# Kernel tuning notes

Measured on AMD Instinct MI355X. Metric: run time of the kernel, lower is better.

## Reference

```python
import jax, jax.numpy as jnp
import numpy as np

N, H, S = 100, 16, 6  # n_subactors, neurons, state_size
B, T = 128, 128


def setup_inputs() -> dict:
    key = jax.random.key(0)
    ks = jax.random.split(key, 12)
    sc = 1.0 / np.sqrt(H)
    inp = {
        "x":   jax.random.normal(ks[0], (B, T, N, S), dtype=jnp.float32),
        # stacked per-subactor GRU weights (torch gate order: r, z, n)
        "Wih": jax.random.uniform(ks[1], (N, 3 * H, S), minval=-sc, maxval=sc, dtype=jnp.float32),
        "Whh": jax.random.uniform(ks[2], (N, 3 * H, H), minval=-sc, maxval=sc, dtype=jnp.float32),
        "bih": jax.random.uniform(ks[3], (N, 3 * H), minval=-sc, maxval=sc, dtype=jnp.float32),
        "bhh": jax.random.uniform(ks[4], (N, 3 * H), minval=-sc, maxval=sc, dtype=jnp.float32),
        # stacked per-subactor MLP weights
        "W1": jax.random.uniform(ks[5], (N, H, H), minval=-sc, maxval=sc, dtype=jnp.float32),
        "b1": jax.random.uniform(ks[6], (N, H), minval=-sc, maxval=sc, dtype=jnp.float32),
        "W2": jax.random.uniform(ks[7], (N, H, H), minval=-sc, maxval=sc, dtype=jnp.float32),
        "b2": jax.random.uniform(ks[8], (N, H), minval=-sc, maxval=sc, dtype=jnp.float32),
        "W3": jax.random.uniform(ks[9], (N, 1, H), minval=-sc, maxval=sc, dtype=jnp.float32),
        "b3": jax.random.uniform(ks[10], (N, 1), minval=-sc, maxval=sc, dtype=jnp.float32),
    }
    return inp


def reference(x, Wih, Whh, bih, bhh, W1, b1, W2, b2, W3, b3):
    b, t, n, s = x.shape
    h = Whh.shape[-1]
    # input projections for all timesteps/subactors at once: [B,T,N,3H]
    xi = jnp.einsum('btns,ngs->btng', x, Wih) + bih

    def step(hprev, xt):  # hprev [B,N,H], xt [B,N,3H]
        hh = jnp.einsum('bnh,ngh->bng', hprev, Whh) + bhh
        xr, xz, xn = jnp.split(xt, 3, axis=-1)
        hr, hz, hn = jnp.split(hh, 3, axis=-1)
        r = jax.nn.sigmoid(xr + hr)
        z = jax.nn.sigmoid(xz + hz)
        nn_ = jnp.tanh(xn + r * hn)
        hnew = (1.0 - z) * nn_ + z * hprev
        return hnew, hnew

    h0 = jnp.zeros((b, n, h), dtype=x.dtype)
    _, hs = jax.lax.scan(step, h0, jnp.moveaxis(xi, 1, 0))  # [T,B,N,H]
    hs = jnp.moveaxis(hs, 0, 1)  # [B,T,N,H]

    y = jax.nn.relu(jnp.einsum('btnh,nkh->btnk', hs, W1) + b1)
    y = jax.nn.relu(jnp.einsum('btnh,nkh->btnk', y, W2) + b2)
    y = jax.nn.relu(jnp.einsum('btnh,nkh->btnk', y, W3) + b3)  # [B,T,N,1]
    # torch: stack over subactors -> [N,B,T,1] then .view(-1, t, nzones)
    return jnp.transpose(y, (2, 0, 1, 3)).reshape(-1, t, n)
```

## Files before the change

### kernel.cpp

```cpp
#include <hip/hip_runtime.h>

namespace {

constexpr int kN = 100;
constexpr int kH = 16;
constexpr int kS = 6;
constexpr int kB = 128;
constexpr int kT = 128;
constexpr int kNS = kN * kS;
constexpr int kXB = kT * kNS;
constexpr float kL2E = 1.44269504088896340736f;

typedef float f32x4 __attribute__((ext_vector_type(4)));
typedef float vf2 __attribute__((ext_vector_type(2)));
typedef short bf16x8 __attribute__((ext_vector_type(8)));

union Frag {
  unsigned u[4];
  bf16x8 v;
};

__device__ __forceinline__ unsigned pkbf(float a, float b) {
  unsigned ua = __builtin_bit_cast(unsigned, a);
  unsigned ub = __builtin_bit_cast(unsigned, b);
  ua += 0x7fffu + ((ua >> 16) & 1u);
  ub += 0x7fffu + ((ub >> 16) & 1u);
  return (ua >> 16) | (ub & 0xffff0000u);
}

__device__ __forceinline__ float rcp_fast(float v) {
  return __builtin_amdgcn_rcpf(v);
}
__device__ __forceinline__ float exp2_fast(float v) {
  return __builtin_amdgcn_exp2f(v);
}
__device__ __forceinline__ vf2 pkfma(vf2 a, vf2 b, vf2 c) {
  return __builtin_elementwise_fma(a, b, c);
}

__device__ __forceinline__ f32x4 mfma16(bf16x8 a, bf16x8 b, f32x4 c) {
  return __builtin_amdgcn_mfma_f32_16x16x32_bf16(a, b, c, 0, 0, 0);
}

__device__ __forceinline__ void mkA(Frag& F, int qt, const float* hrow,
                                    const float* xrow, float sc) {
  F.u[0] = F.u[1] = F.u[2] = F.u[3] = 0u;
  if (hrow) {
    F.u[0] = pkbf(hrow[4 * qt + 0] * sc, hrow[4 * qt + 1] * sc);
    F.u[1] = pkbf(hrow[4 * qt + 2] * sc, hrow[4 * qt + 3] * sc);
  }
  if (xrow && qt < 3) {
    F.u[2] = pkbf(xrow[2 * qt + 0] * sc, xrow[2 * qt + 1] * sc);
  }
}

}

__global__ __launch_bounds__(64) void actor_pk2(
    const float* __restrict__ x, const float* __restrict__ Wih,
    const float* __restrict__ Whh, const float* __restrict__ bih,
    const float* __restrict__ bhh, const float* __restrict__ W1,
    const float* __restrict__ b1, const float* __restrict__ W2,
    const float* __restrict__ b2, const float* __restrict__ W3,
    const float* __restrict__ b3, float* __restrict__ out) {
  const int tid = (int)threadIdx.x;
  const int j = tid & 15;
  const int qt = tid >> 4;
  const int n = (int)blockIdx.x >> 3;
  const int bt = (int)blockIdx.x & 7;

  Frag Ar, Az, Anh, Anx, Ay1, Ay2;
  mkA(Ar, qt, Whh + ((size_t)n * 48 + j) * 16, Wih + ((size_t)n * 48 + j) * 6,
      kL2E);
  mkA(Az, qt, Whh + ((size_t)n * 48 + 16 + j) * 16,
      Wih + ((size_t)n * 48 + 16 + j) * 6, kL2E);
  mkA(Anh, qt, Whh + ((size_t)n * 48 + 32 + j) * 16, nullptr, 2.0f * kL2E);
  mkA(Anx, qt, nullptr, Wih + ((size_t)n * 48 + 32 + j) * 6, 2.0f * kL2E);
  mkA(Ay1, qt, W1 + ((size_t)n * 16 + j) * 16, nullptr, 1.0f);
  mkA(Ay2, qt, W2 + ((size_t)n * 16 + j) * 16, nullptr, 1.0f);

  f32x4 Cbr, Cbz, Cbhn, Cbin, Cb1, Cb2;
  vf2 w301, w323;
#pragma unroll
  for (int r = 0; r < 4; ++r) {
    const int gi = n * 48 + 4 * qt + r;
    Cbr[r] = (bih[gi] + bhh[gi]) * kL2E;
    Cbz[r] = (bih[gi + 16] + bhh[gi + 16]) * kL2E;
    Cbin[r] = bih[gi + 32] * 2.0f * kL2E;
    Cbhn[r] = bhh[gi + 32] * 2.0f * kL2E;
    const int hi = n * 16 + 4 * qt + r;
    Cb1[r] = b1[hi];
    Cb2[r] = b2[hi];
  }
  w301 = (vf2){W3[n * 16 + 4 * qt + 0], W3[n * 16 + 4 * qt + 1]};
  w323 = (vf2){W3[n * 16 + 4 * qt + 2], W3[n * 16 + 4 * qt + 3]};
  const float b3s = b3[n];

  const int b = bt * 16 + j;
  const float* px =
      x + (size_t)b * kXB + (size_t)n * kS + (qt < 3 ? 2 * qt : 0);
  float* outp = out + ((size_t)n * kB + b) * kT;

  float2 xr[4];
#pragma unroll
  for (int i = 0; i < 4; ++i) xr[i] = *(const float2*)(px + (size_t)i * kNS);

  vf2 hp01 = (vf2){0.f, 0.f}, hp23 = (vf2){0.f, 0.f};
  unsigned P0 = 0u, P1 = 0u;

  const f32x4 zero4 = {0.f, 0.f, 0.f, 0.f};
  f32x4 Cy1p = zero4;
  f32x4 Cy2p = zero4;
  float s4[4] = {0.f, 0.f, 0.f, 0.f};

  const vf2 one2 = (vf2){1.f, 1.f};
  const vf2 m2 = (vf2){-2.f, -2.f};
  const vf2 z2 = (vf2){0.f, 0.f};

  auto step = [&](int t, bool doRec, bool doA, bool doB, bool doC) {
    f32x4 Cr, Cz, Chn, Cxn, Cy1n = Cy1p;
    if (t <= kT) {
      const int sl = t & 3;
      Frag Bf;
      Bf.u[0] = P0;
      Bf.u[1] = P1;
      Bf.u[2] = (qt < 3) ? pkbf(xr[sl].x, xr[sl].y) : 0u;
      Bf.u[3] = 0u;
      {
        int tc = t + 4;
        if (tc > kT - 1) tc = kT - 1;
        xr[sl] = *(const float2*)(px + (size_t)tc * kNS);
      }
      if (doRec) {
        Cr = mfma16(Ar.v, Bf.v, Cbr);
        Cz = mfma16(Az.v, Bf.v, Cbz);
        Chn = mfma16(Anh.v, Bf.v, Cbhn);
        Cxn = mfma16(Anx.v, Bf.v, Cbin);
      }
      Cy1n = mfma16(Ay1.v, Bf.v, Cb1);
    }

    if (doB) {
      vf2 a = __builtin_elementwise_max((vf2){Cy2p[0], Cy2p[1]}, z2);
      vf2 c = __builtin_elementwise_max((vf2){Cy2p[2], Cy2p[3]}, z2);
      vf2 p = pkfma(c, w323, a * w301);
      s4[(t - 3) & 3] = p.x + p.y;
    }

    if (doA) {
      vf2 a = __builtin_elementwise_max((vf2){Cy1p[0], Cy1p[1]}, z2);
      vf2 c = __builtin_elementwise_max((vf2){Cy1p[2], Cy1p[3]}, z2);
      Frag By;
      By.u[0] = pkbf(a.x, a.y);
      By.u[1] = pkbf(c.x, c.y);
      By.u[2] = 0u;
      By.u[3] = 0u;
      Cy2p = mfma16(Ay2.v, By.v, Cb2);
    }

    if (doC) {
      float v0 = s4[0], v1 = s4[1], v2 = s4[2], v3 = s4[3];
      v0 += __shfl_xor(v0, 16);
      v1 += __shfl_xor(v1, 16);
      v2 += __shfl_xor(v2, 16);
      v3 += __shfl_xor(v3, 16);
      v0 += __shfl_xor(v0, 32);
      v1 += __shfl_xor(v1, 32);
      v2 += __shfl_xor(v2, 32);
      v3 += __shfl_xor(v3, 32);
      if (qt == 0) {
        float4 o = {fmaxf(v0 + b3s, 0.f), fmaxf(v1 + b3s, 0.f),
                    fmaxf(v2 + b3s, 0.f), fmaxf(v3 + b3s, 0.f)};
        *(float4*)(outp + (t - 6)) = o;
      }
    }

    if (doRec) {
      vf2 cr01 = {Cr[0], Cr[1]}, cr23 = {Cr[2], Cr[3]};
      vf2 cz01 = {Cz[0], Cz[1]}, cz23 = {Cz[2], Cz[3]};
      vf2 chn01 = {Chn[0], Chn[1]}, chn23 = {Chn[2], Chn[3]};
      vf2 cxn01 = {Cxn[0], Cxn[1]}, cxn23 = {Cxn[2], Cxn[3]};

      vf2 er01 = {exp2_fast(-cr01.x), exp2_fast(-cr01.y)};
      vf2 er23 = {exp2_fast(-cr23.x), exp2_fast(-cr23.y)};
      vf2 dr01 = er01 + one2, dr23 = er23 + one2;
      vf2 rr01 = {rcp_fast(dr01.x), rcp_fast(dr01.y)};
      vf2 rr23 = {rcp_fast(dr23.x), rcp_fast(dr23.y)};

      vf2 ez01 = {exp2_fast(-cz01.x), exp2_fast(-cz01.y)};
      vf2 ez23 = {exp2_fast(-cz23.x), exp2_fast(-cz23.y)};
      vf2 dz01 = ez01 + one2, dz23 = ez23 + one2;
      vf2 zz01 = {rcp_fast(dz01.x), rcp_fast(dz01.y)};
      vf2 zz23 = {rcp_fast(dz23.x), rcp_fast(dz23.y)};

      vf2 np01 = pkfma(rr01, chn01, cxn01);
      vf2 np23 = pkfma(rr23, chn23, cxn23);
      vf2 en01 = {exp2_fast(np01.x), exp2_fast(np01.y)};
      vf2 en23 = {exp2_fast(np23.x), exp2_fast(np23.y)};
      vf2 dn01 = en01 + one2, dn23 = en23 + one2;
      vf2 rn01 = {rcp_fast(dn01.x), rcp_fast(dn01.y)};
      vf2 rn23 = {rcp_fast(dn23.x), rcp_fast(dn23.y)};
      vf2 nn01 = pkfma(m2, rn01, one2);
      vf2 nn23 = pkfma(m2, rn23, one2);

      hp01 = pkfma(zz01, hp01 - nn01, nn01);
      hp23 = pkfma(zz23, hp23 - nn23, nn23);
      P0 = pkbf(hp01.x, hp01.y);
      P1 = pkbf(hp23.x, hp23.y);
    }

    Cy1p = Cy1n;
  };

  step(0, true, false, false, false);
  step(1, true, false, false, false);
  step(2, true, true, false, false);
  step(3, true, true, true, false);

  for (int t4 = 4; t4 < kT; t4 += 4) {
    step(t4 + 0, true, true, true, false);
    step(t4 + 1, true, true, true, false);
    step(t4 + 2, true, true, true, true);
    step(t4 + 3, true, true, true, false);
  }

  step(kT, false, true, true, false);
  step(kT + 1, false, true, true, false);
  step(kT + 2, false, false, true, true);
}

extern "C" void kernel_launch(void* const* d_in, const int* in_sizes, int n_in,
                              void* d_out, int out_size, void* d_ws,
                              size_t ws_size, hipStream_t stream) {
  const float* x = (const float*)d_in[0];
  const float* Wih = (const float*)d_in[1];
  const float* Whh = (const float*)d_in[2];
  const float* bih = (const float*)d_in[3];
  const float* bhh = (const float*)d_in[4];
  const float* W1 = (const float*)d_in[5];
  const float* b1 = (const float*)d_in[6];
  const float* W2 = (const float*)d_in[7];
  const float* b2 = (const float*)d_in[8];
  const float* W3 = (const float*)d_in[9];
  const float* b3 = (const float*)d_in[10];
  float* out = (float*)d_out;

  actor_pk2<<<dim3(kN * 8), dim3(64), 0, stream>>>(x, Wih, Whh, bih, bhh, W1,
                                                   b1, W2, b2, W3, b3, out);
}
```

Baseline: 138.3 us.

## Interleave two subactor GRU recurrences per wavefront to hide dependency latency

Each 64-thread block now processes two subactors (n and n+50) for the same batch tile, interleaving their MFMA and gate computations in one unrolled step. The grid drops from 800 to 400 blocks. The aim is to fill the latency of the serial MFMA→exp/rcp→pack chain with independent work from the second recurrence. In exchange it roughly doubles register use and halves the number of concurrently running waves.

```diff
diff --git a/kernel.cpp b/kernel.cpp
--- a/kernel.cpp
+++ b/kernel.cpp
@@ -56,7 +56,7 @@
 
 }
 
-__global__ __launch_bounds__(64) void actor_pk2(
+__global__ __launch_bounds__(64) void actor_dual(
     const float* __restrict__ x, const float* __restrict__ Wih,
     const float* __restrict__ Whh, const float* __restrict__ bih,
     const float* __restrict__ bhh, const float* __restrict__ W1,
@@ -66,150 +66,176 @@
   const int tid = (int)threadIdx.x;
   const int j = tid & 15;
   const int qt = tid >> 4;
-  const int n = (int)blockIdx.x >> 3;
+  const int np = (int)blockIdx.x >> 3;
   const int bt = (int)blockIdx.x & 7;
 
-  Frag Ar, Az, Anh, Anx, Ay1, Ay2;
-  mkA(Ar, qt, Whh + ((size_t)n * 48 + j) * 16, Wih + ((size_t)n * 48 + j) * 6,
-      kL2E);
-  mkA(Az, qt, Whh + ((size_t)n * 48 + 16 + j) * 16,
-      Wih + ((size_t)n * 48 + 16 + j) * 6, kL2E);
-  mkA(Anh, qt, Whh + ((size_t)n * 48 + 32 + j) * 16, nullptr, 2.0f * kL2E);
-  mkA(Anx, qt, nullptr, Wih + ((size_t)n * 48 + 32 + j) * 6, 2.0f * kL2E);
-  mkA(Ay1, qt, W1 + ((size_t)n * 16 + j) * 16, nullptr, 1.0f);
-  mkA(Ay2, qt, W2 + ((size_t)n * 16 + j) * 16, nullptr, 1.0f);
-
-  f32x4 Cbr, Cbz, Cbhn, Cbin, Cb1, Cb2;
-  vf2 w301, w323;
-#pragma unroll
-  for (int r = 0; r < 4; ++r) {
-    const int gi = n * 48 + 4 * qt + r;
-    Cbr[r] = (bih[gi] + bhh[gi]) * kL2E;
-    Cbz[r] = (bih[gi + 16] + bhh[gi + 16]) * kL2E;
-    Cbin[r] = bih[gi + 32] * 2.0f * kL2E;
-    Cbhn[r] = bhh[gi + 32] * 2.0f * kL2E;
-    const int hi = n * 16 + 4 * qt + r;
-    Cb1[r] = b1[hi];
-    Cb2[r] = b2[hi];
-  }
-  w301 = (vf2){W3[n * 16 + 4 * qt + 0], W3[n * 16 + 4 * qt + 1]};
-  w323 = (vf2){W3[n * 16 + 4 * qt + 2], W3[n * 16 + 4 * qt + 3]};
-  const float b3s = b3[n];
-
-  const int b = bt * 16 + j;
-  const float* px =
-      x + (size_t)b * kXB + (size_t)n * kS + (qt < 3 ? 2 * qt : 0);
-  float* outp = out + ((size_t)n * kB + b) * kT;
-
-  float2 xr[4];
-#pragma unroll
-  for (int i = 0; i < 4; ++i) xr[i] = *(const float2*)(px + (size_t)i * kNS);
-
-  vf2 hp01 = (vf2){0.f, 0.f}, hp23 = (vf2){0.f, 0.f};
-  unsigned P0 = 0u, P1 = 0u;
+  Frag Ar[2], Az[2], Anh[2], Anx[2], Ay1[2], Ay2[2];
+  f32x4 Cbr[2], Cbz[2], Cbhn[2], Cbin[2], Cb1[2], Cb2[2];
+  vf2 w301[2], w323[2];
+  float b3s[2];
+  const float* px[2];
+  float* outp[2];
+
+#pragma unroll
+  for (int c = 0; c < 2; ++c) {
+    const int n = np + 50 * c;
+    mkA(Ar[c], qt, Whh + ((size_t)n * 48 + j) * 16,
+        Wih + ((size_t)n * 48 + j) * 6, kL2E);
+    mkA(Az[c], qt, Whh + ((size_t)n * 48 + 16 + j) * 16,
+        Wih + ((size_t)n * 48 + 16 + j) * 6, kL2E);
+    mkA(Anh[c], qt, Whh + ((size_t)n * 48 + 32 + j) * 16, nullptr,
+        2.0f * kL2E);
+    mkA(Anx[c], qt, nullptr, Wih + ((size_t)n * 48 + 32 + j) * 6,
+        2.0f * kL2E);
+    mkA(Ay1[c], qt, W1 + ((size_t)n * 16 + j) * 16, nullptr, 1.0f);
+    mkA(Ay2[c], qt, W2 + ((size_t)n * 16 + j) * 16, nullptr, 1.0f);
+#pragma unroll
+    for (int r = 0; r < 4; ++r) {
+      const int gi = n * 48 + 4 * qt + r;
+      Cbr[c][r] = (bih[gi] + bhh[gi]) * kL2E;
+      Cbz[c][r] = (bih[gi + 16] + bhh[gi + 16]) * kL2E;
+      Cbin[c][r] = bih[gi + 32] * 2.0f * kL2E;
+      Cbhn[c][r] = bhh[gi + 32] * 2.0f * kL2E;
+      const int hi = n * 16 + 4 * qt + r;
+      Cb1[c][r] = b1[hi];
+      Cb2[c][r] = b2[hi];
+    }
+    w301[c] = (vf2){W3[n * 16 + 4 * qt + 0], W3[n * 16 + 4 * qt + 1]};
+    w323[c] = (vf2){W3[n * 16 + 4 * qt + 2], W3[n * 16 + 4 * qt + 3]};
+    b3s[c] = b3[n];
+    const int b = bt * 16 + j;
+    px[c] = x + (size_t)b * kXB + (size_t)n * kS + (qt < 3 ? 2 * qt : 0);
+    outp[c] = out + ((size_t)n * kB + b) * kT;
+  }
+
+  float2 xr[2][4];
+#pragma unroll
+  for (int c = 0; c < 2; ++c)
+#pragma unroll
+    for (int i = 0; i < 4; ++i)
+      xr[c][i] = *(const float2*)(px[c] + (size_t)i * kNS);
+
+  vf2 hp01[2] = {(vf2){0.f, 0.f}, (vf2){0.f, 0.f}};
+  vf2 hp23[2] = {(vf2){0.f, 0.f}, (vf2){0.f, 0.f}};
+  unsigned P0[2] = {0u, 0u}, P1[2] = {0u, 0u};
 
   const f32x4 zero4 = {0.f, 0.f, 0.f, 0.f};
-  f32x4 Cy1p = zero4;
-  f32x4 Cy2p = zero4;
-  float s4[4] = {0.f, 0.f, 0.f, 0.f};
+  f32x4 Cy1p[2] = {zero4, zero4};
+  f32x4 Cy2p[2] = {zero4, zero4};
+  float s4[2][4] = {{0.f, 0.f, 0.f, 0.f}, {0.f, 0.f, 0.f, 0.f}};
 
   const vf2 one2 = (vf2){1.f, 1.f};
   const vf2 m2 = (vf2){-2.f, -2.f};
   const vf2 z2 = (vf2){0.f, 0.f};
 
   auto step = [&](int t, bool doRec, bool doA, bool doB, bool doC) {
-    f32x4 Cr, Cz, Chn, Cxn, Cy1n = Cy1p;
+    f32x4 Cr[2], Cz[2], Chn[2], Cxn[2], Cy1n[2];
+    Cy1n[0] = Cy1p[0];
+    Cy1n[1] = Cy1p[1];
+
     if (t <= kT) {
       const int sl = t & 3;
-      Frag Bf;
-      Bf.u[0] = P0;
-      Bf.u[1] = P1;
-      Bf.u[2] = (qt < 3) ? pkbf(xr[sl].x, xr[sl].y) : 0u;
-      Bf.u[3] = 0u;
-      {
-        int tc = t + 4;
-        if (tc > kT - 1) tc = kT - 1;
-        xr[sl] = *(const float2*)(px + (size_t)tc * kNS);
-      }
-      if (doRec) {
-        Cr = mfma16(Ar.v, Bf.v, Cbr);
-        Cz = mfma16(Az.v, Bf.v, Cbz);
-        Chn = mfma16(Anh.v, Bf.v, Cbhn);
-        Cxn = mfma16(Anx.v, Bf.v, Cbin);
-      }
-      Cy1n = mfma16(Ay1.v, Bf.v, Cb1);
-    }
-
-    if (doB) {
-      vf2 a = __builtin_elementwise_max((vf2){Cy2p[0], Cy2p[1]}, z2);
-      vf2 c = __builtin_elementwise_max((vf2){Cy2p[2], Cy2p[3]}, z2);
-      vf2 p = pkfma(c, w323, a * w301);
-      s4[(t - 3) & 3] = p.x + p.y;
-    }
-
-    if (doA) {
-      vf2 a = __builtin_elementwise_max((vf2){Cy1p[0], Cy1p[1]}, z2);
-      vf2 c = __builtin_elementwise_max((vf2){Cy1p[2], Cy1p[3]}, z2);
-      Frag By;
-      By.u[0] = pkbf(a.x, a.y);
-      By.u[1] = pkbf(c.x, c.y);
-      By.u[2] = 0u;
-      By.u[3] = 0u;
-      Cy2p = mfma16(Ay2.v, By.v, Cb2);
+#pragma unroll
+      for (int c = 0; c < 2; ++c) {
+        Frag Bf;
+        Bf.u[0] = P0[c];
+        Bf.u[1] = P1[c];
+        Bf.u[2] = (qt < 3) ? pkbf(xr[c][sl].x, xr[c][sl].y) : 0u;
+        Bf.u[3] = 0u;
+        {
+          int tc = t + 4;
+          if (tc > kT - 1) tc = kT - 1;
+          xr[c][sl] = *(const float2*)(px[c] + (size_t)tc * kNS);
+        }
+        if (doRec) {
+          Cr[c] = mfma16(Ar[c].v, Bf.v, Cbr[c]);
+          Cz[c] = mfma16(Az[c].v, Bf.v, Cbz[c]);
+          Chn[c] = mfma16(Anh[c].v, Bf.v, Cbhn[c]);
+          Cxn[c] = mfma16(Anx[c].v, Bf.v, Cbin[c]);
+        }
+        Cy1n[c] = mfma16(Ay1[c].v, Bf.v, Cb1[c]);
+      }
+    }
+
+#pragma unroll
+    for (int c = 0; c < 2; ++c) {
+      if (doB) {
+        vf2 a = __builtin_elementwise_max((vf2){Cy2p[c][0], Cy2p[c][1]}, z2);
+        vf2 d = __builtin_elementwise_max((vf2){Cy2p[c][2], Cy2p[c][3]}, z2);
+        vf2 p = pkfma(d, w323[c], a * w301[c]);
+        s4[c][(t - 3) & 3] = p.x + p.y;
+      }
+      if (doA) {
+        vf2 a = __builtin_elementwise_max((vf2){Cy1p[c][0], Cy1p[c][1]}, z2);
+        vf2 d = __builtin_elementwise_max((vf2){Cy1p[c][2], Cy1p[c][3]}, z2);
+        Frag By;
+        By.u[0] = pkbf(a.x, a.y);
+        By.u[1] = pkbf(d.x, d.y);
+        By.u[2] = 0u;
+        By.u[3] = 0u;
+        Cy2p[c] = mfma16(Ay2[c].v, By.v, Cb2[c]);
+      }
     }
 
     if (doC) {
-      float v0 = s4[0], v1 = s4[1], v2 = s4[2], v3 = s4[3];
-      v0 += __shfl_xor(v0, 16);
-      v1 += __shfl_xor(v1, 16);
-      v2 += __shfl_xor(v2, 16);
-      v3 += __shfl_xor(v3, 16);
-      v0 += __shfl_xor(v0, 32);
-      v1 += __shfl_xor(v1, 32);
-      v2 += __shfl_xor(v2, 32);
-      v3 += __shfl_xor(v3, 32);
-      if (qt == 0) {
-        float4 o = {fmaxf(v0 + b3s, 0.f), fmaxf(v1 + b3s, 0.f),
-                    fmaxf(v2 + b3s, 0.f), fmaxf(v3 + b3s, 0.f)};
-        *(float4*)(outp + (t - 6)) = o;
+#pragma unroll
+      for (int c = 0; c < 2; ++c) {
+        float v0 = s4[c][0], v1 = s4[c][1], v2 = s4[c][2], v3 = s4[c][3];
+        v0 += __shfl_xor(v0, 16);
+        v1 += __shfl_xor(v1, 16);
+        v2 += __shfl_xor(v2, 16);
+        v3 += __shfl_xor(v3, 16);
+        v0 += __shfl_xor(v0, 32);
+        v1 += __shfl_xor(v1, 32);
+        v2 += __shfl_xor(v2, 32);
+        v3 += __shfl_xor(v3, 32);
+        if (qt == 0) {
+          float4 o = {fmaxf(v0 + b3s[c], 0.f), fmaxf(v1 + b3s[c], 0.f),
+                      fmaxf(v2 + b3s[c], 0.f), fmaxf(v3 + b3s[c], 0.f)};
+          *(float4*)(outp[c] + (t - 6)) = o;
+        }
       }
     }
 
     if (doRec) {
-      vf2 cr01 = {Cr[0], Cr[1]}, cr23 = {Cr[2], Cr[3]};
-      vf2 cz01 = {Cz[0], Cz[1]}, cz23 = {Cz[2], Cz[3]};
-      vf2 chn01 = {Chn[0], Chn[1]}, chn23 = {Chn[2], Chn[3]};
-      vf2 cxn01 = {Cxn[0], Cxn[1]}, cxn23 = {Cxn[2], Cxn[3]};
-
-      vf2 er01 = {exp2_fast(-cr01.x), exp2_fast(-cr01.y)};
-      vf2 er23 = {exp2_fast(-cr23.x), exp2_fast(-cr23.y)};
-      vf2 dr01 = er01 + one2, dr23 = er23 + one2;
-      vf2 rr01 = {rcp_fast(dr01.x), rcp_fast(dr01.y)};
-      vf2 rr23 = {rcp_fast(dr23.x), rcp_fast(dr23.y)};
-
-      vf2 ez01 = {exp2_fast(-cz01.x), exp2_fast(-cz01.y)};
-      vf2 ez23 = {exp2_fast(-cz23.x), exp2_fast(-cz23.y)};
-      vf2 dz01 = ez01 + one2, dz23 = ez23 + one2;
-      vf2 zz01 = {rcp_fast(dz01.x), rcp_fast(dz01.y)};
-      vf2 zz23 = {rcp_fast(dz23.x), rcp_fast(dz23.y)};
-
-      vf2 np01 = pkfma(rr01, chn01, cxn01);
-      vf2 np23 = pkfma(rr23, chn23, cxn23);
-      vf2 en01 = {exp2_fast(np01.x), exp2_fast(np01.y)};
-      vf2 en23 = {exp2_fast(np23.x), exp2_fast(np23.y)};
-      vf2 dn01 = en01 + one2, dn23 = en23 + one2;
-      vf2 rn01 = {rcp_fast(dn01.x), rcp_fast(dn01.y)};
-      vf2 rn23 = {rcp_fast(dn23.x), rcp_fast(dn23.y)};
-      vf2 nn01 = pkfma(m2, rn01, one2);
-      vf2 nn23 = pkfma(m2, rn23, one2);
-
-      hp01 = pkfma(zz01, hp01 - nn01, nn01);
-      hp23 = pkfma(zz23, hp23 - nn23, nn23);
-      P0 = pkbf(hp01.x, hp01.y);
-      P1 = pkbf(hp23.x, hp23.y);
-    }
-
-    Cy1p = Cy1n;
+#pragma unroll
+      for (int c = 0; c < 2; ++c) {
+        vf2 cr01 = {Cr[c][0], Cr[c][1]}, cr23 = {Cr[c][2], Cr[c][3]};
+        vf2 cz01 = {Cz[c][0], Cz[c][1]}, cz23 = {Cz[c][2], Cz[c][3]};
+        vf2 chn01 = {Chn[c][0], Chn[c][1]}, chn23 = {Chn[c][2], Chn[c][3]};
+        vf2 cxn01 = {Cxn[c][0], Cxn[c][1]}, cxn23 = {Cxn[c][2], Cxn[c][3]};
+
+        vf2 er01 = {exp2_fast(-cr01.x), exp2_fast(-cr01.y)};
+        vf2 er23 = {exp2_fast(-cr23.x), exp2_fast(-cr23.y)};
+        vf2 dr01 = er01 + one2, dr23 = er23 + one2;
+        vf2 rr01 = {rcp_fast(dr01.x), rcp_fast(dr01.y)};
+        vf2 rr23 = {rcp_fast(dr23.x), rcp_fast(dr23.y)};
+
+        vf2 ez01 = {exp2_fast(-cz01.x), exp2_fast(-cz01.y)};
+        vf2 ez23 = {exp2_fast(-cz23.x), exp2_fast(-cz23.y)};
+        vf2 dz01 = ez01 + one2, dz23 = ez23 + one2;
+        vf2 zz01 = {rcp_fast(dz01.x), rcp_fast(dz01.y)};
+        vf2 zz23 = {rcp_fast(dz23.x), rcp_fast(dz23.y)};
+
+        vf2 np01 = pkfma(rr01, chn01, cxn01);
+        vf2 np23 = pkfma(rr23, chn23, cxn23);
+        vf2 en01 = {exp2_fast(np01.x), exp2_fast(np01.y)};
+        vf2 en23 = {exp2_fast(np23.x), exp2_fast(np23.y)};
+        vf2 dn01 = en01 + one2, dn23 = en23 + one2;
+        vf2 rn01 = {rcp_fast(dn01.x), rcp_fast(dn01.y)};
+        vf2 rn23 = {rcp_fast(dn23.x), rcp_fast(dn23.y)};
+        vf2 nn01 = pkfma(m2, rn01, one2);
+        vf2 nn23 = pkfma(m2, rn23, one2);
+
+        hp01[c] = pkfma(zz01, hp01[c] - nn01, nn01);
+        hp23[c] = pkfma(zz23, hp23[c] - nn23, nn23);
+        P0[c] = pkbf(hp01[c].x, hp01[c].y);
+        P1[c] = pkbf(hp23[c].x, hp23[c].y);
+      }
+    }
+
+    Cy1p[0] = Cy1n[0];
+    Cy1p[1] = Cy1n[1];
   };
 
   step(0, true, false, false, false);
@@ -245,6 +271,6 @@
   const float* b3 = (const float*)d_in[10];
   float* out = (float*)d_out;
 
-  actor_pk2<<<dim3(kN * 8), dim3(64), 0, stream>>>(x, Wih, Whh, bih, bhh, W1,
-                                                   b1, W2, b2, W3, b3, out);
-}
+  actor_dual<<<dim3(50 * 8), dim3(64), 0, stream>>>(x, Wih, Whh, bih, bhh, W1,
+                                                    b1, W2, b2, W3, b3, out);
+}
```

After: 179.7 us. +29.9%, slower.

## Split GRU recurrence and MLP head into producer/consumer wavefronts via LDS

Applied to the files above, without the earlier changes.

The single-wave kernel becomes a two-wave block. Wave 0 runs only the serial GRU recurrence over chunks of 8 timesteps and writes the packed bf16 hidden states into a 16-slot LDS ring. Wave 1 consumes the previous chunk and runs the three-layer MLP and the output reduction. A block barrier is placed after each chunk. The aim is to take the MLP MFMAs and shuffles off the latency-critical recurrence path so the two waves can overlap, and to prefetch x 8 steps ahead with double buffering. The cost is a barrier every 8 steps, LDS traffic, and twice as many threads per block.

```diff
diff --git a/kernel.cpp b/kernel.cpp
--- a/kernel.cpp
+++ b/kernel.cpp
@@ -13,6 +13,7 @@
 
 typedef float f32x4 __attribute__((ext_vector_type(4)));
 typedef float vf2 __attribute__((ext_vector_type(2)));
+typedef unsigned u32x2 __attribute__((ext_vector_type(2)));
 typedef short bf16x8 __attribute__((ext_vector_type(8)));
 
 union Frag {
@@ -56,177 +57,184 @@
 
 }
 
-__global__ __launch_bounds__(64) void actor_pk2(
+__global__ __launch_bounds__(128) void actor_pc(
     const float* __restrict__ x, const float* __restrict__ Wih,
     const float* __restrict__ Whh, const float* __restrict__ bih,
     const float* __restrict__ bhh, const float* __restrict__ W1,
     const float* __restrict__ b1, const float* __restrict__ W2,
     const float* __restrict__ b2, const float* __restrict__ W3,
     const float* __restrict__ b3, float* __restrict__ out) {
+  __shared__ unsigned shh[16 * 128];
+
   const int tid = (int)threadIdx.x;
-  const int j = tid & 15;
-  const int qt = tid >> 4;
+  const int wid = tid >> 6;
+  const int lane = tid & 63;
+  const int j = lane & 15;
+  const int qt = lane >> 4;
   const int n = (int)blockIdx.x >> 3;
   const int bt = (int)blockIdx.x & 7;
-
-  Frag Ar, Az, Anh, Anx, Ay1, Ay2;
-  mkA(Ar, qt, Whh + ((size_t)n * 48 + j) * 16, Wih + ((size_t)n * 48 + j) * 6,
-      kL2E);
-  mkA(Az, qt, Whh + ((size_t)n * 48 + 16 + j) * 16,
-      Wih + ((size_t)n * 48 + 16 + j) * 6, kL2E);
-  mkA(Anh, qt, Whh + ((size_t)n * 48 + 32 + j) * 16, nullptr, 2.0f * kL2E);
-  mkA(Anx, qt, nullptr, Wih + ((size_t)n * 48 + 32 + j) * 6, 2.0f * kL2E);
-  mkA(Ay1, qt, W1 + ((size_t)n * 16 + j) * 16, nullptr, 1.0f);
-  mkA(Ay2, qt, W2 + ((size_t)n * 16 + j) * 16, nullptr, 1.0f);
-
-  f32x4 Cbr, Cbz, Cbhn, Cbin, Cb1, Cb2;
-  vf2 w301, w323;
-#pragma unroll
-  for (int r = 0; r < 4; ++r) {
-    const int gi = n * 48 + 4 * qt + r;
-    Cbr[r] = (bih[gi] + bhh[gi]) * kL2E;
-    Cbz[r] = (bih[gi + 16] + bhh[gi + 16]) * kL2E;
-    Cbin[r] = bih[gi + 32] * 2.0f * kL2E;
-    Cbhn[r] = bhh[gi + 32] * 2.0f * kL2E;
-    const int hi = n * 16 + 4 * qt + r;
-    Cb1[r] = b1[hi];
-    Cb2[r] = b2[hi];
-  }
-  w301 = (vf2){W3[n * 16 + 4 * qt + 0], W3[n * 16 + 4 * qt + 1]};
-  w323 = (vf2){W3[n * 16 + 4 * qt + 2], W3[n * 16 + 4 * qt + 3]};
-  const float b3s = b3[n];
-
   const int b = bt * 16 + j;
+
+  Frag Ar, Az, Anh, Anx;
+  f32x4 Cbr, Cbz, Cbhn, Cbin;
   const float* px =
       x + (size_t)b * kXB + (size_t)n * kS + (qt < 3 ? 2 * qt : 0);
+
+  Frag Ay1, Ay2;
+  f32x4 Cb1, Cb2;
+  vf2 w301, w323;
+  float b3s;
   float* outp = out + ((size_t)n * kB + b) * kT;
 
-  float2 xr[4];
-#pragma unroll
-  for (int i = 0; i < 4; ++i) xr[i] = *(const float2*)(px + (size_t)i * kNS);
-
+  if (wid == 0) {
+    mkA(Ar, qt, Whh + ((size_t)n * 48 + j) * 16,
+        Wih + ((size_t)n * 48 + j) * 6, kL2E);
+    mkA(Az, qt, Whh + ((size_t)n * 48 + 16 + j) * 16,
+        Wih + ((size_t)n * 48 + 16 + j) * 6, kL2E);
+    mkA(Anh, qt, Whh + ((size_t)n * 48 + 32 + j) * 16, nullptr, 2.0f * kL2E);
+    mkA(Anx, qt, nullptr, Wih + ((size_t)n * 48 + 32 + j) * 6, 2.0f * kL2E);
+#pragma unroll
+    for (int r = 0; r < 4; ++r) {
+      const int gi = n * 48 + 4 * qt + r;
+      Cbr[r] = (bih[gi] + bhh[gi]) * kL2E;
+      Cbz[r] = (bih[gi + 16] + bhh[gi + 16]) * kL2E;
+      Cbin[r] = bih[gi + 32] * 2.0f * kL2E;
+      Cbhn[r] = bhh[gi + 32] * 2.0f * kL2E;
+    }
+  } else {
+    mkA(Ay1, qt, W1 + ((size_t)n * 16 + j) * 16, nullptr, 1.0f);
+    mkA(Ay2, qt, W2 + ((size_t)n * 16 + j) * 16, nullptr, 1.0f);
+#pragma unroll
+    for (int r = 0; r < 4; ++r) {
+      const int hi = n * 16 + 4 * qt + r;
+      Cb1[r] = b1[hi];
+      Cb2[r] = b2[hi];
+    }
+    w301 = (vf2){W3[n * 16 + 4 * qt + 0], W3[n * 16 + 4 * qt + 1]};
+    w323 = (vf2){W3[n * 16 + 4 * qt + 2], W3[n * 16 + 4 * qt + 3]};
+    b3s = b3[n];
+  }
+
+  float2 xbuf[2][8];
+  if (wid == 0) {
+#pragma unroll
+    for (int i = 0; i < 8; ++i)
+      xbuf[0][i] = *(const float2*)(px + (size_t)i * kNS);
+  }
   vf2 hp01 = (vf2){0.f, 0.f}, hp23 = (vf2){0.f, 0.f};
   unsigned P0 = 0u, P1 = 0u;
-
-  const f32x4 zero4 = {0.f, 0.f, 0.f, 0.f};
-  f32x4 Cy1p = zero4;
-  f32x4 Cy2p = zero4;
-  float s4[4] = {0.f, 0.f, 0.f, 0.f};
 
   const vf2 one2 = (vf2){1.f, 1.f};
   const vf2 m2 = (vf2){-2.f, -2.f};
   const vf2 z2 = (vf2){0.f, 0.f};
 
-  auto step = [&](int t, bool doRec, bool doA, bool doB, bool doC) {
-    f32x4 Cr, Cz, Chn, Cxn, Cy1n = Cy1p;
-    if (t <= kT) {
-      const int sl = t & 3;
-      Frag Bf;
-      Bf.u[0] = P0;
-      Bf.u[1] = P1;
-      Bf.u[2] = (qt < 3) ? pkbf(xr[sl].x, xr[sl].y) : 0u;
-      Bf.u[3] = 0u;
-      {
-        int tc = t + 4;
-        if (tc > kT - 1) tc = kT - 1;
-        xr[sl] = *(const float2*)(px + (size_t)tc * kNS);
+  for (int w = 0; w <= 16; ++w) {
+    if (wid == 0) {
+      if (w < 16) {
+        const int nb = (w + 1) & 1;
+#pragma unroll
+        for (int i = 0; i < 8; ++i) {
+          int tc = 8 * (w + 1) + i;
+          if (tc > kT - 1) tc = kT - 1;
+          xbuf[nb][i] = *(const float2*)(px + (size_t)tc * kNS);
+        }
+        const int cb = w & 1;
+#pragma unroll
+        for (int k = 0; k < 8; ++k) {
+          const int t = 8 * w + k;
+          Frag Bf;
+          Bf.u[0] = P0;
+          Bf.u[1] = P1;
+          Bf.u[2] = pkbf(xbuf[cb][k].x, xbuf[cb][k].y);
+          Bf.u[3] = 0u;
+
+          const f32x4 Cr = mfma16(Ar.v, Bf.v, Cbr);
+          const f32x4 Cz = mfma16(Az.v, Bf.v, Cbz);
+          const f32x4 Chn = mfma16(Anh.v, Bf.v, Cbhn);
+          const f32x4 Cxn = mfma16(Anx.v, Bf.v, Cbin);
+
+          vf2 cr01 = {Cr[0], Cr[1]}, cr23 = {Cr[2], Cr[3]};
+          vf2 cz01 = {Cz[0], Cz[1]}, cz23 = {Cz[2], Cz[3]};
+          vf2 chn01 = {Chn[0], Chn[1]}, chn23 = {Chn[2], Chn[3]};
+          vf2 cxn01 = {Cxn[0], Cxn[1]}, cxn23 = {Cxn[2], Cxn[3]};
+
+          vf2 er01 = {exp2_fast(-cr01.x), exp2_fast(-cr01.y)};
+          vf2 er23 = {exp2_fast(-cr23.x), exp2_fast(-cr23.y)};
+          vf2 dr01 = er01 + one2, dr23 = er23 + one2;
+          vf2 rr01 = {rcp_fast(dr01.x), rcp_fast(dr01.y)};
+          vf2 rr23 = {rcp_fast(dr23.x), rcp_fast(dr23.y)};
+
+          vf2 ez01 = {exp2_fast(-cz01.x), exp2_fast(-cz01.y)};
+          vf2 ez23 = {exp2_fast(-cz23.x), exp2_fast(-cz23.y)};
+          vf2 dz01 = ez01 + one2, dz23 = ez23 + one2;
+          vf2 zz01 = {rcp_fast(dz01.x), rcp_fast(dz01.y)};
+          vf2 zz23 = {rcp_fast(dz23.x), rcp_fast(dz23.y)};
+
+          vf2 np01 = pkfma(rr01, chn01, cxn01);
+          vf2 np23 = pkfma(rr23, chn23, cxn23);
+          vf2 en01 = {exp2_fast(np01.x), exp2_fast(np01.y)};
+          vf2 en23 = {exp2_fast(np23.x), exp2_fast(np23.y)};
+          vf2 dn01 = en01 + one2, dn23 = en23 + one2;
+          vf2 rn01 = {rcp_fast(dn01.x), rcp_fast(dn01.y)};
+          vf2 rn23 = {rcp_fast(dn23.x), rcp_fast(dn23.y)};
+          vf2 nn01 = pkfma(m2, rn01, one2);
+          vf2 nn23 = pkfma(m2, rn23, one2);
+
+          hp01 = pkfma(zz01, hp01 - nn01, nn01);
+          hp23 = pkfma(zz23, hp23 - nn23, nn23);
+          P0 = pkbf(hp01.x, hp01.y);
+          P1 = pkbf(hp23.x, hp23.y);
+
+          *(u32x2*)&shh[(t & 15) * 128 + lane * 2] = (u32x2){P0, P1};
+        }
       }
-      if (doRec) {
-        Cr = mfma16(Ar.v, Bf.v, Cbr);
-        Cz = mfma16(Az.v, Bf.v, Cbz);
-        Chn = mfma16(Anh.v, Bf.v, Cbhn);
-        Cxn = mfma16(Anx.v, Bf.v, Cbin);
-      }
-      Cy1n = mfma16(Ay1.v, Bf.v, Cb1);
-    }
-
-    if (doB) {
-      vf2 a = __builtin_elementwise_max((vf2){Cy2p[0], Cy2p[1]}, z2);
-      vf2 c = __builtin_elementwise_max((vf2){Cy2p[2], Cy2p[3]}, z2);
-      vf2 p = pkfma(c, w323, a * w301);
-      s4[(t - 3) & 3] = p.x + p.y;
-    }
-
-    if (doA) {
-      vf2 a = __builtin_elementwise_max((vf2){Cy1p[0], Cy1p[1]}, z2);
-      vf2 c = __builtin_elementwise_max((vf2){Cy1p[2], Cy1p[3]}, z2);
-      Frag By;
-      By.u[0] = pkbf(a.x, a.y);
-      By.u[1] = pkbf(c.x, c.y);
-      By.u[2] = 0u;
-      By.u[3] = 0u;
-      Cy2p = mfma16(Ay2.v, By.v, Cb2);
-    }
-
-    if (doC) {
-      float v0 = s4[0], v1 = s4[1], v2 = s4[2], v3 = s4[3];
-      v0 += __shfl_xor(v0, 16);
-      v1 += __shfl_xor(v1, 16);
-      v2 += __shfl_xor(v2, 16);
-      v3 += __shfl_xor(v3, 16);
-      v0 += __shfl_xor(v0, 32);
-      v1 += __shfl_xor(v1, 32);
-      v2 += __shfl_xor(v2, 32);
-      v3 += __shfl_xor(v3, 32);
-      if (qt == 0) {
-        float4 o = {fmaxf(v0 + b3s, 0.f), fmaxf(v1 + b3s, 0.f),
-                    fmaxf(v2 + b3s, 0.f), fmaxf(v3 + b3s, 0.f)};
-        *(float4*)(outp + (t - 6)) = o;
+    } else {
+      if (w >= 1) {
+        const int t0 = 8 * (w - 1);
+        float s4[4];
+#pragma unroll
+        for (int k = 0; k < 8; ++k) {
+          const int t = t0 + k;
+          const u32x2 P = *(const u32x2*)&shh[(t & 15) * 128 + lane * 2];
+          Frag Bh;
+          Bh.u[0] = P.x;
+          Bh.u[1] = P.y;
+          Bh.u[2] = 0u;
+          Bh.u[3] = 0u;
+          const f32x4 Cy1 = mfma16(Ay1.v, Bh.v, Cb1);
+          vf2 a = __builtin_elementwise_max((vf2){Cy1[0], Cy1[1]}, z2);
+          vf2 c = __builtin_elementwise_max((vf2){Cy1[2], Cy1[3]}, z2);
+          Frag By;
+          By.u[0] = pkbf(a.x, a.y);
+          By.u[1] = pkbf(c.x, c.y);
+          By.u[2] = 0u;
+          By.u[3] = 0u;
+          const f32x4 Cy2 = mfma16(Ay2.v, By.v, Cb2);
+          vf2 a2 = __builtin_elementwise_max((vf2){Cy2[0], Cy2[1]}, z2);
+          vf2 c2 = __builtin_elementwise_max((vf2){Cy2[2], Cy2[3]}, z2);
+          vf2 p = pkfma(c2, w323, a2 * w301);
+          s4[k & 3] = p.x + p.y;
+          if ((k & 3) == 3) {
+            float v0 = s4[0], v1 = s4[1], v2 = s4[2], v3 = s4[3];
+            v0 += __shfl_xor(v0, 16);
+            v1 += __shfl_xor(v1, 16);
+            v2 += __shfl_xor(v2, 16);
+            v3 += __shfl_xor(v3, 16);
+            v0 += __shfl_xor(v0, 32);
+            v1 += __shfl_xor(v1, 32);
+            v2 += __shfl_xor(v2, 32);
+            v3 += __shfl_xor(v3, 32);
+            if (qt == 0) {
+              float4 o = {fmaxf(v0 + b3s, 0.f), fmaxf(v1 + b3s, 0.f),
+                          fmaxf(v2 + b3s, 0.f), fmaxf(v3 + b3s, 0.f)};
+              *(float4*)(outp + (t - 3)) = o;
+            }
+          }
+        }
       }
     }
-
-    if (doRec) {
-      vf2 cr01 = {Cr[0], Cr[1]}, cr23 = {Cr[2], Cr[3]};
-      vf2 cz01 = {Cz[0], Cz[1]}, cz23 = {Cz[2], Cz[3]};
-      vf2 chn01 = {Chn[0], Chn[1]}, chn23 = {Chn[2], Chn[3]};
-      vf2 cxn01 = {Cxn[0], Cxn[1]}, cxn23 = {Cxn[2], Cxn[3]};
-
-      vf2 er01 = {exp2_fast(-cr01.x), exp2_fast(-cr01.y)};
-      vf2 er23 = {exp2_fast(-cr23.x), exp2_fast(-cr23.y)};
-      vf2 dr01 = er01 + one2, dr23 = er23 + one2;
-      vf2 rr01 = {rcp_fast(dr01.x), rcp_fast(dr01.y)};
-      vf2 rr23 = {rcp_fast(dr23.x), rcp_fast(dr23.y)};
-
-      vf2 ez01 = {exp2_fast(-cz01.x), exp2_fast(-cz01.y)};
-      vf2 ez23 = {exp2_fast(-cz23.x), exp2_fast(-cz23.y)};
-      vf2 dz01 = ez01 + one2, dz23 = ez23 + one2;
-      vf2 zz01 = {rcp_fast(dz01.x), rcp_fast(dz01.y)};
-      vf2 zz23 = {rcp_fast(dz23.x), rcp_fast(dz23.y)};
-
-      vf2 np01 = pkfma(rr01, chn01, cxn01);
-      vf2 np23 = pkfma(rr23, chn23, cxn23);
-      vf2 en01 = {exp2_fast(np01.x), exp2_fast(np01.y)};
-      vf2 en23 = {exp2_fast(np23.x), exp2_fast(np23.y)};
-      vf2 dn01 = en01 + one2, dn23 = en23 + one2;
-      vf2 rn01 = {rcp_fast(dn01.x), rcp_fast(dn01.y)};
-      vf2 rn23 = {rcp_fast(dn23.x), rcp_fast(dn23.y)};
-      vf2 nn01 = pkfma(m2, rn01, one2);
-      vf2 nn23 = pkfma(m2, rn23, one2);
-
-      hp01 = pkfma(zz01, hp01 - nn01, nn01);
-      hp23 = pkfma(zz23, hp23 - nn23, nn23);
-      P0 = pkbf(hp01.x, hp01.y);
-      P1 = pkbf(hp23.x, hp23.y);
-    }
-
-    Cy1p = Cy1n;
-  };
-
-  step(0, true, false, false, false);
-  step(1, true, false, false, false);
-  step(2, true, true, false, false);
-  step(3, true, true, true, false);
-
-  for (int t4 = 4; t4 < kT; t4 += 4) {
-    step(t4 + 0, true, true, true, false);
-    step(t4 + 1, true, true, true, false);
-    step(t4 + 2, true, true, true, true);
-    step(t4 + 3, true, true, true, false);
-  }
-
-  step(kT, false, true, true, false);
-  step(kT + 1, false, true, true, false);
-  step(kT + 2, false, false, true, true);
+    if (w < 16) __syncthreads();
+  }
 }
 
 extern "C" void kernel_launch(void* const* d_in, const int* in_sizes, int n_in,
@@ -245,6 +253,6 @@
   const float* b3 = (const float*)d_in[10];
   float* out = (float*)d_out;
 
-  actor_pk2<<<dim3(kN * 8), dim3(64), 0, stream>>>(x, Wih, Whh, bih, bhh, W1,
+  actor_pc<<<dim3(kN * 8), dim3(128), 0, stream>>>(x, Wih, Whh, bih, bhh, W1,
                                                    b1, W2, b2, W3, b3, out);
 }
```

Result: slower. 162.8 us (+17.7%).
